# Kernel optimization log

Hardware: AMD Instinct MI355X
Metric: run time of the kernel (lower is better)

## Reference

```python
import jax, jax.numpy as jnp
import numpy as np

NC = 4
X = Y = Z = 64
IMG_SHAPE = (96, 96, 96)
SPAN = 2          # FILTER_SIZE = [5,5,5]
NUM_ITER = 4
DIL = 2           # DILATION = 2.0
SMOOTH_DISTANCE_INIT = 0.3
PRIOR_DISTANCE_INIT = 0.3


def _ind(d):
    # mirrors _get_ind from the torch code
    return (d, 0) if d > 0 else (0, -d)


def _sl(a, b):
    # slice(a, -b) with -0 -> None, mirrors _negative
    return slice(a, -b if b else None)


def _offsets():
    for dx in range(-SPAN, SPAN + 1):
        for dy in range(-SPAN, SPAN + 1):
            for dz in range(-SPAN, SPAN + 1):
                yield dx, dy, dz


def _lin_resize_axis(x, axis, out):
    # 1D linear interpolation matching torch align_corners=True
    n = x.shape[axis]
    if out == n:
        return x
    pos = jnp.arange(out, dtype=x.dtype) * ((n - 1) / (out - 1))
    i0 = jnp.clip(jnp.floor(pos).astype(jnp.int32), 0, n - 1)
    i1 = jnp.clip(i0 + 1, 0, n - 1)
    w = pos - i0.astype(x.dtype)
    shp = [1] * x.ndim
    shp[axis] = out
    w = w.reshape(shp)
    return jnp.take(x, i0, axis=axis) * (1 - w) + jnp.take(x, i1, axis=axis) * w


def _resize3d(x, out_sz):
    # trilinear, align_corners=True, separable over the 3 spatial axes of [b,c,X,Y,Z]
    for ax, o in zip((2, 3, 4), out_sz):
        x = _lin_resize_axis(x, ax, o)
    return x


def _smooth_gaussian(feats):
    # feats: [b, c, X, Y, Z] -> gaussian [b, 5,5,5, X, Y, Z]
    b = feats.shape[0]
    sp = feats.shape[2:]
    g = jnp.zeros((b, 5, 5, 5) + sp, feats.dtype)
    for dx, dy, dz in _offsets():
        dx1, dx2 = _ind(dx); dy1, dy2 = _ind(dy); dz1, dz2 = _ind(dz)
        a = feats[:, :, _sl(dx1, dx2), _sl(dy1, dy2), _sl(dz1, dz2)]
        c = feats[:, :, _sl(dx2, dx1), _sl(dy2, dy1), _sl(dz2, dz1)]
        e = jnp.exp(-0.5 * jnp.sum((a - c) ** 2, axis=1))
        g = g.at[:, dx + SPAN, dy + SPAN, dz + SPAN,
                 _sl(dx2, dx1), _sl(dy2, dy1), _sl(dz2, dz1)].set(e)
    return g


def _prior_gaussian(f1, f2):
    # f1, f2: [b, c, x, y, z] (already downsampled) -> [b, 5,5,5, x, y, z]
    b = f1.shape[0]
    sp = f1.shape[2:]
    g = jnp.zeros((b, 5, 5, 5) + sp, f1.dtype)
    for dx, dy, dz in _offsets():
        dx1, dx2 = _ind(dx); dy1, dy2 = _ind(dy); dz1, dz2 = _ind(dz)
        a = f1[:, :, _sl(dx2, dx1), _sl(dy2, dy1), _sl(dz2, dz1)]
        c = f2[:, :, _sl(dx1, dx2), _sl(dy1, dy2), _sl(dz1, dz2)]
        e = jnp.exp(-0.5 * jnp.sum((a - c) ** 2, axis=1))
        g = g.at[:, dx + SPAN, dy + SPAN, dz + SPAN,
                 _sl(dx2, dx1), _sl(dy2, dy1), _sl(dz2, dz1)].set(e)
    return g


def _message(p, g):
    # p: [b, nc, x, y, z]; g: [b, 5,5,5, x, y, z]
    out = jnp.zeros_like(p)
    for dx, dy, dz in _offsets():
        dx1, dx2 = _ind(dx); dy1, dy2 = _ind(dy); dz1, dz2 = _ind(dz)
        a = p[:, :, _sl(dx1, dx2), _sl(dy1, dy2), _sl(dz1, dz2)]
        w = g[:, None, dx + SPAN, dy + SPAN, dz + SPAN,
              _sl(dx2, dx1), _sl(dy2, dy1), _sl(dz2, dz1)]
        out = out.at[:, :, _sl(dx2, dx1), _sl(dy2, dy1), _sl(dz2, dz1)].add(a * w)
    return out


def setup_inputs() -> dict:
    key = jax.random.key(0)
    ks = jax.random.split(key, 6)
    unary = jax.random.normal(ks[0], (1, NC, X, Y, Z), jnp.float32)
    img = jax.random.normal(ks[1], (1, 2, X, Y, Z), jnp.float32)
    atlas = jax.random.normal(ks[2], (1, 2, X, Y, Z), jnp.float32)
    atlas_label = jax.random.uniform(ks[3], (1, X, Y, Z, NC), jnp.float32)
    patch_start = jax.random.randint(ks[4], (1, 3), 0, 32, jnp.int32)
    return {
        "unary": unary,
        "img": img,
        "atlas": atlas,
        "atlas_label": atlas_label,
        "patch_start": patch_start,
        "smooth_norm": jnp.array([1.0 / SMOOTH_DISTANCE_INIT], jnp.float32),
        "smooth_weight": jnp.ones((NC,), jnp.float32),
        "prior_norm": jnp.array([1.0 / PRIOR_DISTANCE_INIT], jnp.float32),
        "prior_weight": jnp.ones(IMG_SHAPE, jnp.float32),
        "compat_w": jnp.eye(NC, dtype=jnp.float32),
    }


def reference(unary, img, atlas, atlas_label, patch_start,
              smooth_norm, smooth_weight, prior_norm, prior_weight, compat_w):
    b, nc, x, y, z = unary.shape
    ds = (x // DIL, y // DIL, z // DIL)  # floor(in*0.5) == ceil(in/2) for even dims

    # similarity kernels
    sg = _smooth_gaussian(img * smooth_norm)                      # [b,5,5,5,x,y,z]
    f1 = _resize3d(img * prior_norm, ds)
    f2 = _resize3d(atlas * prior_norm, ds)
    pg = _prior_gaussian(f1, f2)                                  # [b,5,5,5,x/2,y/2,z/2]

    # prior message is independent of q_values: compute once
    al = jnp.transpose(atlas_label, (0, 4, 1, 2, 3))              # [b,nc,x,y,z]
    al_ds = _resize3d(al, ds)
    pm = _resize3d(_message(al_ds, pg), (x, y, z))                # [b,nc,x,y,z]
    pw = jax.lax.dynamic_slice(
        prior_weight,
        (patch_start[0, 0], patch_start[0, 1], patch_start[0, 2]),
        (x, y, z))
    prior_term = pw[None, None] * pm

    q = unary
    for _ in range(NUM_ITER):
        p = jax.nn.softmax(q, axis=1)
        sm = _message(p, sg)
        pred = smooth_weight[None, :, None, None, None] * sm + prior_term
        q = unary + jnp.einsum('oc,bcxyz->boxyz', compat_w, pred)  # 1x1x1 compat conv
    return q
```

## Files before the change

### kernel.cpp

```cpp
#include <hip/hip_runtime.h>

#define NN 64
#define N3 (64*64*64)
#define DS 32
#define DS3 (32*32*32)

#define LOG2E 1.4426950408889634f
#define FSCALE 0.8493218002880191f

typedef _Float16 h2  __attribute__((ext_vector_type(2)));
typedef __fp16   h2f __attribute__((ext_vector_type(2)));

__device__ __forceinline__ float fexp2(float x) { return __builtin_amdgcn_exp2f(x); }

__device__ __forceinline__ h2 u2h(unsigned u) { union { unsigned u; h2 h; } c; c.u = u; return c.h; }
__device__ __forceinline__ unsigned h2u(h2 h) { union { unsigned u; h2 h; } c; c.h = h; return c.u; }
__device__ __forceinline__ h2 pkh(float a, float b) {
    union { h2f a; h2 b; } c; c.a = __builtin_amdgcn_cvt_pkrtz(a, b); return c.b;
}
__device__ __forceinline__ float fdot2(h2 a, h2 b) {
    union { h2 h; h2f f; } ca, cb; ca.h = a; cb.h = b;
    return __builtin_amdgcn_fdot2(ca.f, cb.f, 0.0f, false);
}

__device__ __forceinline__ void axw(int j, float scale, int nmax, int& i0, int& i1, float& w) {
    float pos = (float)j * scale;
    int f = (int)floorf(pos);
    if (f < 0) f = 0;
    if (f > nmax) f = nmax;
    i0 = f;
    i1 = (f + 1 <= nmax) ? f + 1 : nmax;
    w = pos - (float)f;
}


__global__ __launch_bounds__(128) void k_downsample(
    const float* __restrict__ img, const float* __restrict__ atlas,
    const float* __restrict__ alabel, const float* __restrict__ pnorm,
    unsigned* __restrict__ f1pk, uint4* __restrict__ nb)
{
    int idx = blockIdx.x * 128 + threadIdx.x;
    int z = idx & 31, y = (idx >> 5) & 31, x = idx >> 10;

    const float scale = 63.0f / 31.0f;
    int x0,x1,y0,y1,z0,z1; float wx,wy,wz;
    axw(x, scale, 63, x0, x1, wx);
    axw(y, scale, 63, y0, y1, wy);
    axw(z, scale, 63, z0, z1, wz);

    float w000=(1-wx)*(1-wy)*(1-wz), w001=(1-wx)*(1-wy)*wz;
    float w010=(1-wx)*wy*(1-wz),     w011=(1-wx)*wy*wz;
    float w100=wx*(1-wy)*(1-wz),     w101=wx*(1-wy)*wz;
    float w110=wx*wy*(1-wz),         w111=wx*wy*wz;

    int c000=(x0*NN+y0)*NN+z0, c001=(x0*NN+y0)*NN+z1;
    int c010=(x0*NN+y1)*NN+z0, c011=(x0*NN+y1)*NN+z1;
    int c100=(x1*NN+y0)*NN+z0, c101=(x1*NN+y0)*NN+z1;
    int c110=(x1*NN+y1)*NN+z0, c111=(x1*NN+y1)*NN+z1;

    auto tri = [&](const float* p) -> float {
        return p[c000]*w000 + p[c001]*w001 + p[c010]*w010 + p[c011]*w011
             + p[c100]*w100 + p[c101]*w101 + p[c110]*w110 + p[c111]*w111;
    };
    float pnf = pnorm[0] * FSCALE;
    f1pk[idx] = h2u(pkh(pnf*tri(img), pnf*tri(img + N3)));

    auto tril = [&](int c) -> float {
        return alabel[c000*4+c]*w000 + alabel[c001*4+c]*w001 + alabel[c010*4+c]*w010 + alabel[c011*4+c]*w011
             + alabel[c100*4+c]*w100 + alabel[c101*4+c]*w101 + alabel[c110*4+c]*w110 + alabel[c111*4+c]*w111;
    };
    nb[idx] = make_uint4(h2u(pkh(pnf*tri(atlas), pnf*tri(atlas + N3))),
                         h2u(pkh(tril(0), tril(1))),
                         h2u(pkh(tril(2), tril(3))), 0u);
}

__global__ __launch_bounds__(128) void k_prior_msg(
    const unsigned* __restrict__ f1pk, const uint4* __restrict__ nb,
    float4* __restrict__ pm)
{
    int idx = blockIdx.x * 128 + threadIdx.x;
    int z = idx & 31, y = (idx >> 5) & 31, x = idx >> 10;

    h2 ncf = -u2h(f1pk[idx]);
    float a0=0.f, a1=0.f, a2=0.f, a3=0.f;
    for (int dx = -2; dx <= 2; ++dx) {
        int xx = x + dx; if ((unsigned)xx >= DS) continue;
        for (int dy = -2; dy <= 2; ++dy) {
            int yy = y + dy; if ((unsigned)yy >= DS) continue;
            int base = (xx*DS + yy)*DS;
            #pragma unroll
            for (int dz = -2; dz <= 2; ++dz) {
                int zz = z + dz; if ((unsigned)zz >= DS) continue;
                uint4 v = nb[base + zz];
                h2 d = u2h(v.x) + ncf;
                float t = fdot2(d, d);
                float w = fexp2(-t);
                h2 l01 = u2h(v.y), l23 = u2h(v.z);
                a0 += w*(float)l01.x; a1 += w*(float)l01.y;
                a2 += w*(float)l23.x; a3 += w*(float)l23.y;
            }
        }
    }
    pm[idx] = make_float4(a0, a1, a2, a3);
}

__global__ void k_upsample_prior(const float4* __restrict__ pm, const float* __restrict__ pweight,
                                 const int* __restrict__ pstart, float4* __restrict__ prior4)
{
    int idx = blockIdx.x * blockDim.x + threadIdx.x;
    if (idx >= N3) return;
    int z = idx & 63, y = (idx >> 6) & 63, x = idx >> 12;

    const float scale = 31.0f / 63.0f;
    int x0,x1,y0,y1,z0,z1; float wx,wy,wz;
    axw(x, scale, 31, x0, x1, wx);
    axw(y, scale, 31, y0, y1, wy);
    axw(z, scale, 31, z0, z1, wz);

    float w000=(1-wx)*(1-wy)*(1-wz), w001=(1-wx)*(1-wy)*wz;
    float w010=(1-wx)*wy*(1-wz),     w011=(1-wx)*wy*wz;
    float w100=wx*(1-wy)*(1-wz),     w101=wx*(1-wy)*wz;
    float w110=wx*wy*(1-wz),         w111=wx*wy*wz;

    float4 p000=pm[(x0*DS+y0)*DS+z0], p001=pm[(x0*DS+y0)*DS+z1];
    float4 p010=pm[(x0*DS+y1)*DS+z0], p011=pm[(x0*DS+y1)*DS+z1];
    float4 p100=pm[(x1*DS+y0)*DS+z0], p101=pm[(x1*DS+y0)*DS+z1];
    float4 p110=pm[(x1*DS+y1)*DS+z0], p111=pm[(x1*DS+y1)*DS+z1];

    float4 r;
    r.x = w000*p000.x + w001*p001.x + w010*p010.x + w011*p011.x + w100*p100.x + w101*p101.x + w110*p110.x + w111*p111.x;
    r.y = w000*p000.y + w001*p001.y + w010*p010.y + w011*p011.y + w100*p100.y + w101*p101.y + w110*p110.y + w111*p111.y;
    r.z = w000*p000.z + w001*p001.z + w010*p010.z + w011*p011.z + w100*p100.z + w101*p101.z + w110*p110.z + w111*p111.z;
    r.w = w000*p000.w + w001*p001.w + w010*p010.w + w011*p011.w + w100*p100.w + w101*p101.w + w110*p110.w + w111*p111.w;

    float w = pweight[(pstart[0]+x)*96*96 + (pstart[1]+y)*96 + (pstart[2]+z)];
    r.x *= w; r.y *= w; r.z *= w; r.w *= w;
    prior4[idx] = r;
}


#define TXD 8
#define TYD 8
#define TZR 8
#define RZ 2
#define TZD (TZR*RZ)
#define HX 12
#define HY 12
#define HZ 20
#define PZ 22

__global__ __launch_bounds__(512, 2) void k_iter(
    const float* __restrict__ qin,
    const float* __restrict__ unary,
    const float* __restrict__ img,
    const float* __restrict__ snorm,
    const float* __restrict__ sweight,
    const float* __restrict__ compat,
    const float4* __restrict__ prior4,
    float* __restrict__ qout)
{
    __shared__ __align__(16) uint2    pS[HX][HY][PZ];
    __shared__ __align__(8)  unsigned fS[HX][HY][PZ];

    const int tzg = threadIdx.x, ty = threadIdx.y, tx = threadIdx.z;
    const int x0b = blockIdx.z * TXD, y0b = blockIdx.y * TYD, z0b = blockIdx.x * TZD;
    const int tid = (tx*TYD + ty)*TZR + tzg;
    const float sc = snorm[0] * FSCALE;

    #pragma unroll
    for (int rr = 0; rr < 6; ++rr) {
        int i = tid + rr*512;
        if (i < HX*HY*HZ) {
            int lz = i % HZ; int r = i / HZ;
            int ly = r % HY; int lx = r / HY;
            int gx = x0b + lx - 2, gy = y0b + ly - 2, gz = z0b + lz - 2;
            uint2 pu = make_uint2(0u, 0u);
            unsigned fu = 0u;
            if ((unsigned)gx < NN && (unsigned)gy < NN && (unsigned)gz < NN) {
                int g = (gx*NN + gy)*NN + gz;
                float q0 = qin[g], q1 = qin[g+N3], q2 = qin[g+2*N3], q3 = qin[g+3*N3];
                float m = fmaxf(fmaxf(q0,q1), fmaxf(q2,q3));
                float e0 = fexp2((q0-m)*LOG2E);
                float e1 = fexp2((q1-m)*LOG2E);
                float e2 = fexp2((q2-m)*LOG2E);
                float e3 = fexp2((q3-m)*LOG2E);
                float inv = 1.0f/(e0+e1+e2+e3);
                pu = make_uint2(h2u(pkh(e0*inv, e1*inv)), h2u(pkh(e2*inv, e3*inv)));
                fu = h2u(pkh(img[g]*sc, img[g+N3]*sc));
            }
            pS[lx][ly][lz] = pu;
            fS[lx][ly][lz] = fu;
        }
    }

    const int tz0 = tzg * RZ;
    const int g = ((x0b+tx)*NN + (y0b+ty))*NN + z0b + tz0;
    float4 pr0 = prior4[g], pr1 = prior4[g+1];
    float2 un0 = *(const float2*)(unary + 0*N3 + g);
    float2 un1 = *(const float2*)(unary + 1*N3 + g);
    float2 un2 = *(const float2*)(unary + 2*N3 + g);
    float2 un3 = *(const float2*)(unary + 3*N3 + g);
    float sw0 = sweight[0], sw1 = sweight[1], sw2 = sweight[2], sw3 = sweight[3];
    float cw[16];
    #pragma unroll
    for (int k = 0; k < 16; ++k) cw[k] = compat[k];

    __syncthreads();

    h2 ncf0 = -u2h(fS[tx+2][ty+2][tz0+2]);
    h2 ncf1 = -u2h(fS[tx+2][ty+2][tz0+3]);

    float4 acc0 = make_float4(0.f,0.f,0.f,0.f);
    float4 acc1 = make_float4(0.f,0.f,0.f,0.f);

    for (int dx = 0; dx < 5; ++dx) {
        #pragma unroll
        for (int dy = 0; dy < 5; ++dy) {
            const uint4* pp = reinterpret_cast<const uint4*>(&pS[tx+dx][ty+dy][tz0]);
            const uint2* fp = reinterpret_cast<const uint2*>(&fS[tx+dx][ty+dy][tz0]);
            uint4 qa = pp[0], qb = pp[1], qc = pp[2];
            uint2 fa = fp[0], fb = fp[1], fc = fp[2];

            unsigned fz[6]  = { fa.x, fa.y, fb.x, fb.y, fc.x, fc.y };
            unsigned p01[6] = { qa.x, qa.z, qb.x, qb.z, qc.x, qc.z };
            unsigned p23[6] = { qa.y, qa.w, qb.y, qb.w, qc.y, qc.w };

            #pragma unroll
            for (int dz = 0; dz < 5; ++dz) {
                {
                    h2 d = u2h(fz[dz]) + ncf0;
                    float t = fdot2(d, d);
                    float w = fexp2(-t);
                    h2 a = u2h(p01[dz]), b = u2h(p23[dz]);
                    acc0.x += w*(float)a.x; acc0.y += w*(float)a.y;
                    acc0.z += w*(float)b.x; acc0.w += w*(float)b.y;
                }
                {
                    h2 d = u2h(fz[dz+1]) + ncf1;
                    float t = fdot2(d, d);
                    float w = fexp2(-t);
                    h2 a = u2h(p01[dz+1]), b = u2h(p23[dz+1]);
                    acc1.x += w*(float)a.x; acc1.y += w*(float)a.y;
                    acc1.z += w*(float)b.x; acc1.w += w*(float)b.y;
                }
            }
        }
    }

    float p0, p1, p2, p3;
    float r00, r10, r20, r30, r01, r11, r21, r31;
    p0 = sw0*acc0.x + pr0.x; p1 = sw1*acc0.y + pr0.y; p2 = sw2*acc0.z + pr0.z; p3 = sw3*acc0.w + pr0.w;
    r00 = un0.x + cw[0]*p0  + cw[1]*p1  + cw[2]*p2  + cw[3]*p3;
    r10 = un1.x + cw[4]*p0  + cw[5]*p1  + cw[6]*p2  + cw[7]*p3;
    r20 = un2.x + cw[8]*p0  + cw[9]*p1  + cw[10]*p2 + cw[11]*p3;
    r30 = un3.x + cw[12]*p0 + cw[13]*p1 + cw[14]*p2 + cw[15]*p3;
    p0 = sw0*acc1.x + pr1.x; p1 = sw1*acc1.y + pr1.y; p2 = sw2*acc1.z + pr1.z; p3 = sw3*acc1.w + pr1.w;
    r01 = un0.y + cw[0]*p0  + cw[1]*p1  + cw[2]*p2  + cw[3]*p3;
    r11 = un1.y + cw[4]*p0  + cw[5]*p1  + cw[6]*p2  + cw[7]*p3;
    r21 = un2.y + cw[8]*p0  + cw[9]*p1  + cw[10]*p2 + cw[11]*p3;
    r31 = un3.y + cw[12]*p0 + cw[13]*p1 + cw[14]*p2 + cw[15]*p3;

    *(float2*)(qout + 0*N3 + g) = make_float2(r00, r01);
    *(float2*)(qout + 1*N3 + g) = make_float2(r10, r11);
    *(float2*)(qout + 2*N3 + g) = make_float2(r20, r21);
    *(float2*)(qout + 3*N3 + g) = make_float2(r30, r31);
}


extern "C" void kernel_launch(void* const* d_in, const int* in_sizes, int n_in,
                              void* d_out, int out_size, void* d_ws, size_t ws_size,
                              hipStream_t stream)
{
    const float* unary   = (const float*)d_in[0];
    const float* img     = (const float*)d_in[1];
    const float* atlas   = (const float*)d_in[2];
    const float* alabel  = (const float*)d_in[3];
    const int*   pstart  = (const int*)d_in[4];
    const float* snorm   = (const float*)d_in[5];
    const float* sweight = (const float*)d_in[6];
    const float* pnorm   = (const float*)d_in[7];
    const float* pweight = (const float*)d_in[8];
    const float* compat  = (const float*)d_in[9];
    float* out = (float*)d_out;
    float* ws  = (float*)d_ws;

    float*    prior4 = ws;
    float*    qtmp   = ws + 4*N3;
    unsigned* f1pk   = (unsigned*)(ws + 8*N3);
    uint4*    nbuf   = (uint4*)(f1pk + DS3);
    float*    pm32   = (float*)(nbuf + DS3);

    k_downsample<<<DS3/128, 128, 0, stream>>>(img, atlas, alabel, pnorm, f1pk, nbuf);
    k_prior_msg<<<DS3/128, 128, 0, stream>>>(f1pk, nbuf, (float4*)pm32);
    k_upsample_prior<<<N3/256, 256, 0, stream>>>((const float4*)pm32, pweight, pstart,
                                                 (float4*)prior4);

    dim3 grid(NN/TZD, NN/TYD, NN/TXD), block(TZR, TYD, TXD);
    k_iter<<<grid, block, 0, stream>>>(unary, unary, img, snorm, sweight, compat, (const float4*)prior4, qtmp);
    k_iter<<<grid, block, 0, stream>>>(qtmp,  unary, img, snorm, sweight, compat, (const float4*)prior4, out);
    k_iter<<<grid, block, 0, stream>>>(out,   unary, img, snorm, sweight, compat, (const float4*)prior4, qtmp);
    k_iter<<<grid, block, 0, stream>>>(qtmp,  unary, img, snorm, sweight, compat, (const float4*)prior4, out);
}
```

Measured before the change: 102.7 us.

## Split stencil across two thread halves, fuse prior upsampling, interleave q layout

Each iter block now has 1024 threads. The 25 (dx,dy) stencil rows are split between two thread halves, and the partial sums are reduced through shared memory, so more waves can hide latency. The separate prior upsample kernel is removed: one half of the threads recomputes the trilinear upsample and the patch weight inline in every iteration, using that half's otherwise idle time. Intermediate q buffers switch to an interleaved float4-per-voxel layout so softmax loads and stores become single vector accesses. The cost is the prior recomputed four times, an extra barrier and reduction, and higher register and LDS pressure at 1024 threads.

```diff
diff --git a/kernel.cpp b/kernel.cpp
--- a/kernel.cpp
+++ b/kernel.cpp
@@ -104,40 +104,6 @@
     pm[idx] = make_float4(a0, a1, a2, a3);
 }
 
-__global__ void k_upsample_prior(const float4* __restrict__ pm, const float* __restrict__ pweight,
-                                 const int* __restrict__ pstart, float4* __restrict__ prior4)
-{
-    int idx = blockIdx.x * blockDim.x + threadIdx.x;
-    if (idx >= N3) return;
-    int z = idx & 63, y = (idx >> 6) & 63, x = idx >> 12;
-
-    const float scale = 31.0f / 63.0f;
-    int x0,x1,y0,y1,z0,z1; float wx,wy,wz;
-    axw(x, scale, 31, x0, x1, wx);
-    axw(y, scale, 31, y0, y1, wy);
-    axw(z, scale, 31, z0, z1, wz);
-
-    float w000=(1-wx)*(1-wy)*(1-wz), w001=(1-wx)*(1-wy)*wz;
-    float w010=(1-wx)*wy*(1-wz),     w011=(1-wx)*wy*wz;
-    float w100=wx*(1-wy)*(1-wz),     w101=wx*(1-wy)*wz;
-    float w110=wx*wy*(1-wz),         w111=wx*wy*wz;
-
-    float4 p000=pm[(x0*DS+y0)*DS+z0], p001=pm[(x0*DS+y0)*DS+z1];
-    float4 p010=pm[(x0*DS+y1)*DS+z0], p011=pm[(x0*DS+y1)*DS+z1];
-    float4 p100=pm[(x1*DS+y0)*DS+z0], p101=pm[(x1*DS+y0)*DS+z1];
-    float4 p110=pm[(x1*DS+y1)*DS+z0], p111=pm[(x1*DS+y1)*DS+z1];
-
-    float4 r;
-    r.x = w000*p000.x + w001*p001.x + w010*p010.x + w011*p011.x + w100*p100.x + w101*p101.x + w110*p110.x + w111*p111.x;
-    r.y = w000*p000.y + w001*p001.y + w010*p010.y + w011*p011.y + w100*p100.y + w101*p101.y + w110*p110.y + w111*p111.y;
-    r.z = w000*p000.z + w001*p001.z + w010*p010.z + w011*p011.z + w100*p100.z + w101*p101.z + w110*p110.z + w111*p111.z;
-    r.w = w000*p000.w + w001*p001.w + w010*p010.w + w011*p011.w + w100*p100.w + w101*p101.w + w110*p110.w + w111*p111.w;
-
-    float w = pweight[(pstart[0]+x)*96*96 + (pstart[1]+y)*96 + (pstart[2]+z)];
-    r.x *= w; r.y *= w; r.z *= w; r.w *= w;
-    prior4[idx] = r;
-}
-
 
 #define TXD 8
 #define TYD 8
@@ -149,27 +115,32 @@
 #define HZ 20
 #define PZ 22
 
-__global__ __launch_bounds__(512, 2) void k_iter(
+template<bool QV_IN, bool QV_OUT>
+__global__ __launch_bounds__(1024, 4) void k_iter(
     const float* __restrict__ qin,
     const float* __restrict__ unary,
     const float* __restrict__ img,
     const float* __restrict__ snorm,
     const float* __restrict__ sweight,
     const float* __restrict__ compat,
-    const float4* __restrict__ prior4,
+    const float4* __restrict__ pm,
+    const float* __restrict__ pweight,
+    const int* __restrict__ pstart,
     float* __restrict__ qout)
 {
     __shared__ __align__(16) uint2    pS[HX][HY][PZ];
     __shared__ __align__(8)  unsigned fS[HX][HY][PZ];
-
-    const int tzg = threadIdx.x, ty = threadIdx.y, tx = threadIdx.z;
+    __shared__ __align__(16) float4   accS[TXD*TYD*TZR][2];
+
+    const int tzg = threadIdx.x, ty = threadIdx.y;
+    const int tx = threadIdx.z & 7, s = threadIdx.z >> 3;
     const int x0b = blockIdx.z * TXD, y0b = blockIdx.y * TYD, z0b = blockIdx.x * TZD;
-    const int tid = (tx*TYD + ty)*TZR + tzg;
+    const int tid = threadIdx.x + TZR*threadIdx.y + TZR*TYD*threadIdx.z;
     const float sc = snorm[0] * FSCALE;
 
     #pragma unroll
-    for (int rr = 0; rr < 6; ++rr) {
-        int i = tid + rr*512;
+    for (int rr = 0; rr < 3; ++rr) {
+        int i = tid + rr*1024;
         if (i < HX*HY*HZ) {
             int lz = i % HZ; int r = i / HZ;
             int ly = r % HY; int lx = r / HY;
@@ -178,7 +149,13 @@
             unsigned fu = 0u;
             if ((unsigned)gx < NN && (unsigned)gy < NN && (unsigned)gz < NN) {
                 int g = (gx*NN + gy)*NN + gz;
-                float q0 = qin[g], q1 = qin[g+N3], q2 = qin[g+2*N3], q3 = qin[g+3*N3];
+                float q0, q1, q2, q3;
+                if (QV_IN) {
+                    float4 qv = reinterpret_cast<const float4*>(qin)[g];
+                    q0 = qv.x; q1 = qv.y; q2 = qv.z; q3 = qv.w;
+                } else {
+                    q0 = qin[g]; q1 = qin[g+N3]; q2 = qin[g+2*N3]; q3 = qin[g+3*N3];
+                }
                 float m = fmaxf(fmaxf(q0,q1), fmaxf(q2,q3));
                 float e0 = fexp2((q0-m)*LOG2E);
                 float e1 = fexp2((q1-m)*LOG2E);
@@ -194,16 +171,43 @@
     }
 
     const int tz0 = tzg * RZ;
-    const int g = ((x0b+tx)*NN + (y0b+ty))*NN + z0b + tz0;
-    float4 pr0 = prior4[g], pr1 = prior4[g+1];
-    float2 un0 = *(const float2*)(unary + 0*N3 + g);
-    float2 un1 = *(const float2*)(unary + 1*N3 + g);
-    float2 un2 = *(const float2*)(unary + 2*N3 + g);
-    float2 un3 = *(const float2*)(unary + 3*N3 + g);
-    float sw0 = sweight[0], sw1 = sweight[1], sw2 = sweight[2], sw3 = sweight[3];
-    float cw[16];
-    #pragma unroll
-    for (int k = 0; k < 16; ++k) cw[k] = compat[k];
+    const int gx = x0b + tx, gy = y0b + ty, gz = z0b + tz0;
+
+    float4 pr0 = make_float4(0.f,0.f,0.f,0.f), pr1 = make_float4(0.f,0.f,0.f,0.f);
+    if (s == 1) {
+        const float S13 = 31.0f / 63.0f;
+        float posx = (float)gx * S13; int xc0 = (int)posx; float wxf = posx - (float)xc0;
+        int xc1 = xc0 < 31 ? xc0+1 : 31;
+        float posy = (float)gy * S13; int yc0 = (int)posy; float wyf = posy - (float)yc0;
+        int yc1 = yc0 < 31 ? yc0+1 : 31;
+        int r00i = (xc0*DS+yc0)*DS, r01i = (xc0*DS+yc1)*DS;
+        int r10i = (xc1*DS+yc0)*DS, r11i = (xc1*DS+yc1)*DS;
+        auto upz = [&](int gzv) -> float4 {
+            float posz = (float)gzv * S13; int zc0 = (int)posz; float wzf = posz - (float)zc0;
+            int zc1 = zc0 < 31 ? zc0+1 : 31;
+            float4 p000 = pm[r00i+zc0], p001 = pm[r00i+zc1];
+            float4 p010 = pm[r01i+zc0], p011 = pm[r01i+zc1];
+            float4 p100 = pm[r10i+zc0], p101 = pm[r10i+zc1];
+            float4 p110 = pm[r11i+zc0], p111 = pm[r11i+zc1];
+            float w000=(1-wxf)*(1-wyf)*(1-wzf), w001=(1-wxf)*(1-wyf)*wzf;
+            float w010=(1-wxf)*wyf*(1-wzf),     w011=(1-wxf)*wyf*wzf;
+            float w100=wxf*(1-wyf)*(1-wzf),     w101=wxf*(1-wyf)*wzf;
+            float w110=wxf*wyf*(1-wzf),         w111=wxf*wyf*wzf;
+            float4 r;
+            r.x = w000*p000.x + w001*p001.x + w010*p010.x + w011*p011.x + w100*p100.x + w101*p101.x + w110*p110.x + w111*p111.x;
+            r.y = w000*p000.y + w001*p001.y + w010*p010.y + w011*p011.y + w100*p100.y + w101*p101.y + w110*p110.y + w111*p111.y;
+            r.z = w000*p000.z + w001*p001.z + w010*p010.z + w011*p011.z + w100*p100.z + w101*p101.z + w110*p110.z + w111*p111.z;
+            r.w = w000*p000.w + w001*p001.w + w010*p010.w + w011*p011.w + w100*p100.w + w101*p101.w + w110*p110.w + w111*p111.w;
+            return r;
+        };
+        pr0 = upz(gz);
+        pr1 = upz(gz+1);
+        int ps0 = pstart[0], ps1 = pstart[1], ps2 = pstart[2];
+        int pwbase = (ps0+gx)*96*96 + (ps1+gy)*96 + ps2 + gz;
+        float pwa = pweight[pwbase], pwb = pweight[pwbase+1];
+        pr0.x *= pwa; pr0.y *= pwa; pr0.z *= pwa; pr0.w *= pwa;
+        pr1.x *= pwb; pr1.y *= pwb; pr1.z *= pwb; pr1.w *= pwb;
+    }
 
     __syncthreads();
 
@@ -213,57 +217,83 @@
     float4 acc0 = make_float4(0.f,0.f,0.f,0.f);
     float4 acc1 = make_float4(0.f,0.f,0.f,0.f);
 
-    for (int dx = 0; dx < 5; ++dx) {
+    for (int p = s; p < 25; p += 2) {
+        int dx = p / 5, dy = p - dx*5;
+        const uint4* pp = reinterpret_cast<const uint4*>(&pS[tx+dx][ty+dy][tz0]);
+        const uint2* fp = reinterpret_cast<const uint2*>(&fS[tx+dx][ty+dy][tz0]);
+        uint4 qa = pp[0], qb = pp[1], qc = pp[2];
+        uint2 fa = fp[0], fb = fp[1], fc = fp[2];
+
+        unsigned fz[6]  = { fa.x, fa.y, fb.x, fb.y, fc.x, fc.y };
+        unsigned p01[6] = { qa.x, qa.z, qb.x, qb.z, qc.x, qc.z };
+        unsigned p23[6] = { qa.y, qa.w, qb.y, qb.w, qc.y, qc.w };
+
         #pragma unroll
-        for (int dy = 0; dy < 5; ++dy) {
-            const uint4* pp = reinterpret_cast<const uint4*>(&pS[tx+dx][ty+dy][tz0]);
-            const uint2* fp = reinterpret_cast<const uint2*>(&fS[tx+dx][ty+dy][tz0]);
-            uint4 qa = pp[0], qb = pp[1], qc = pp[2];
-            uint2 fa = fp[0], fb = fp[1], fc = fp[2];
-
-            unsigned fz[6]  = { fa.x, fa.y, fb.x, fb.y, fc.x, fc.y };
-            unsigned p01[6] = { qa.x, qa.z, qb.x, qb.z, qc.x, qc.z };
-            unsigned p23[6] = { qa.y, qa.w, qb.y, qb.w, qc.y, qc.w };
-
-            #pragma unroll
-            for (int dz = 0; dz < 5; ++dz) {
-                {
-                    h2 d = u2h(fz[dz]) + ncf0;
-                    float t = fdot2(d, d);
-                    float w = fexp2(-t);
-                    h2 a = u2h(p01[dz]), b = u2h(p23[dz]);
-                    acc0.x += w*(float)a.x; acc0.y += w*(float)a.y;
-                    acc0.z += w*(float)b.x; acc0.w += w*(float)b.y;
-                }
-                {
-                    h2 d = u2h(fz[dz+1]) + ncf1;
-                    float t = fdot2(d, d);
-                    float w = fexp2(-t);
-                    h2 a = u2h(p01[dz+1]), b = u2h(p23[dz+1]);
-                    acc1.x += w*(float)a.x; acc1.y += w*(float)a.y;
-                    acc1.z += w*(float)b.x; acc1.w += w*(float)b.y;
-                }
+        for (int dz = 0; dz < 5; ++dz) {
+            {
+                h2 d = u2h(fz[dz]) + ncf0;
+                float t = fdot2(d, d);
+                float w = fexp2(-t);
+                h2 a = u2h(p01[dz]), b = u2h(p23[dz]);
+                acc0.x += w*(float)a.x; acc0.y += w*(float)a.y;
+                acc0.z += w*(float)b.x; acc0.w += w*(float)b.y;
+            }
+            {
+                h2 d = u2h(fz[dz+1]) + ncf1;
+                float t = fdot2(d, d);
+                float w = fexp2(-t);
+                h2 a = u2h(p01[dz+1]), b = u2h(p23[dz+1]);
+                acc1.x += w*(float)a.x; acc1.y += w*(float)a.y;
+                acc1.z += w*(float)b.x; acc1.w += w*(float)b.y;
             }
         }
     }
 
-    float p0, p1, p2, p3;
-    float r00, r10, r20, r30, r01, r11, r21, r31;
-    p0 = sw0*acc0.x + pr0.x; p1 = sw1*acc0.y + pr0.y; p2 = sw2*acc0.z + pr0.z; p3 = sw3*acc0.w + pr0.w;
-    r00 = un0.x + cw[0]*p0  + cw[1]*p1  + cw[2]*p2  + cw[3]*p3;
-    r10 = un1.x + cw[4]*p0  + cw[5]*p1  + cw[6]*p2  + cw[7]*p3;
-    r20 = un2.x + cw[8]*p0  + cw[9]*p1  + cw[10]*p2 + cw[11]*p3;
-    r30 = un3.x + cw[12]*p0 + cw[13]*p1 + cw[14]*p2 + cw[15]*p3;
-    p0 = sw0*acc1.x + pr1.x; p1 = sw1*acc1.y + pr1.y; p2 = sw2*acc1.z + pr1.z; p3 = sw3*acc1.w + pr1.w;
-    r01 = un0.y + cw[0]*p0  + cw[1]*p1  + cw[2]*p2  + cw[3]*p3;
-    r11 = un1.y + cw[4]*p0  + cw[5]*p1  + cw[6]*p2  + cw[7]*p3;
-    r21 = un2.y + cw[8]*p0  + cw[9]*p1  + cw[10]*p2 + cw[11]*p3;
-    r31 = un3.y + cw[12]*p0 + cw[13]*p1 + cw[14]*p2 + cw[15]*p3;
-
-    *(float2*)(qout + 0*N3 + g) = make_float2(r00, r01);
-    *(float2*)(qout + 1*N3 + g) = make_float2(r10, r11);
-    *(float2*)(qout + 2*N3 + g) = make_float2(r20, r21);
-    *(float2*)(qout + 3*N3 + g) = make_float2(r30, r31);
+    const int pid = (tx*TYD + ty)*TZR + tzg;
+    if (s == 0) {
+        accS[pid][0] = acc0;
+        accS[pid][1] = acc1;
+    }
+    __syncthreads();
+
+    if (s == 1) {
+        float4 o0 = accS[pid][0], o1 = accS[pid][1];
+        acc0.x += o0.x; acc0.y += o0.y; acc0.z += o0.z; acc0.w += o0.w;
+        acc1.x += o1.x; acc1.y += o1.y; acc1.z += o1.z; acc1.w += o1.w;
+
+        const int g = (gx*NN + gy)*NN + gz;
+        float2 un0 = *(const float2*)(unary + 0*N3 + g);
+        float2 un1 = *(const float2*)(unary + 1*N3 + g);
+        float2 un2 = *(const float2*)(unary + 2*N3 + g);
+        float2 un3 = *(const float2*)(unary + 3*N3 + g);
+        float sw0 = sweight[0], sw1 = sweight[1], sw2 = sweight[2], sw3 = sweight[3];
+        float cw[16];
+        #pragma unroll
+        for (int k = 0; k < 16; ++k) cw[k] = compat[k];
+
+        float p0, p1, p2, p3;
+        float r00, r10, r20, r30, r01, r11, r21, r31;
+        p0 = sw0*acc0.x + pr0.x; p1 = sw1*acc0.y + pr0.y; p2 = sw2*acc0.z + pr0.z; p3 = sw3*acc0.w + pr0.w;
+        r00 = un0.x + cw[0]*p0  + cw[1]*p1  + cw[2]*p2  + cw[3]*p3;
+        r10 = un1.x + cw[4]*p0  + cw[5]*p1  + cw[6]*p2  + cw[7]*p3;
+        r20 = un2.x + cw[8]*p0  + cw[9]*p1  + cw[10]*p2 + cw[11]*p3;
+        r30 = un3.x + cw[12]*p0 + cw[13]*p1 + cw[14]*p2 + cw[15]*p3;
+        p0 = sw0*acc1.x + pr1.x; p1 = sw1*acc1.y + pr1.y; p2 = sw2*acc1.z + pr1.z; p3 = sw3*acc1.w + pr1.w;
+        r01 = un0.y + cw[0]*p0  + cw[1]*p1  + cw[2]*p2  + cw[3]*p3;
+        r11 = un1.y + cw[4]*p0  + cw[5]*p1  + cw[6]*p2  + cw[7]*p3;
+        r21 = un2.y + cw[8]*p0  + cw[9]*p1  + cw[10]*p2 + cw[11]*p3;
+        r31 = un3.y + cw[12]*p0 + cw[13]*p1 + cw[14]*p2 + cw[15]*p3;
+
+        if (QV_OUT) {
+            reinterpret_cast<float4*>(qout)[g]   = make_float4(r00, r10, r20, r30);
+            reinterpret_cast<float4*>(qout)[g+1] = make_float4(r01, r11, r21, r31);
+        } else {
+            *(float2*)(qout + 0*N3 + g) = make_float2(r00, r01);
+            *(float2*)(qout + 1*N3 + g) = make_float2(r10, r11);
+            *(float2*)(qout + 2*N3 + g) = make_float2(r20, r21);
+            *(float2*)(qout + 3*N3 + g) = make_float2(r30, r31);
+        }
+    }
 }
 
 
@@ -284,20 +314,18 @@
     float* out = (float*)d_out;
     float* ws  = (float*)d_ws;
 
-    float*    prior4 = ws;
-    float*    qtmp   = ws + 4*N3;
-    unsigned* f1pk   = (unsigned*)(ws + 8*N3);
-    uint4*    nbuf   = (uint4*)(f1pk + DS3);
-    float*    pm32   = (float*)(nbuf + DS3);
+    float*    qA   = ws;
+    float*    qB   = ws + 4*N3;
+    unsigned* f1pk = (unsigned*)(ws + 8*N3);
+    uint4*    nbuf = (uint4*)(f1pk + DS3);
+    float4*   pm   = (float4*)(nbuf + DS3);
 
     k_downsample<<<DS3/128, 128, 0, stream>>>(img, atlas, alabel, pnorm, f1pk, nbuf);
-    k_prior_msg<<<DS3/128, 128, 0, stream>>>(f1pk, nbuf, (float4*)pm32);
-    k_upsample_prior<<<N3/256, 256, 0, stream>>>((const float4*)pm32, pweight, pstart,
-                                                 (float4*)prior4);
-
-    dim3 grid(NN/TZD, NN/TYD, NN/TXD), block(TZR, TYD, TXD);
-    k_iter<<<grid, block, 0, stream>>>(unary, unary, img, snorm, sweight, compat, (const float4*)prior4, qtmp);
-    k_iter<<<grid, block, 0, stream>>>(qtmp,  unary, img, snorm, sweight, compat, (const float4*)prior4, out);
-    k_iter<<<grid, block, 0, stream>>>(out,   unary, img, snorm, sweight, compat, (const float4*)prior4, qtmp);
-    k_iter<<<grid, block, 0, stream>>>(qtmp,  unary, img, snorm, sweight, compat, (const float4*)prior4, out);
-}
+    k_prior_msg<<<DS3/128, 128, 0, stream>>>(f1pk, nbuf, pm);
+
+    dim3 grid(NN/TZD, NN/TYD, NN/TXD), block(TZR, TYD, 16);
+    k_iter<false,true><<<grid, block, 0, stream>>>(unary, unary, img, snorm, sweight, compat, pm, pweight, pstart, qA);
+    k_iter<true, true><<<grid, block, 0, stream>>>(qA,    unary, img, snorm, sweight, compat, pm, pweight, pstart, qB);
+    k_iter<true, true><<<grid, block, 0, stream>>>(qB,    unary, img, snorm, sweight, compat, pm, pweight, pstart, qA);
+    k_iter<true,false><<<grid, block, 0, stream>>>(qA,    unary, img, snorm, sweight, compat, pm, pweight, pstart, out);
+}
```

Result: faster. 95.58 us (-6.9%).
